# Performance work log

Measured on AMD Instinct MI355X. Metric: run time of the kernel, lower is better.

## Reference

```python
import jax, jax.numpy as jnp
import numpy as np

B, N, D = 4, 1024, 512
H, Dv, Dq = 8, 64, 64
NUM_BUCKETS = 64
LN_EPS = 1e-5


def setup_inputs() -> dict:
    key = jax.random.key(0)
    ks = jax.random.split(key, 10)
    x = jax.random.normal(ks[0], (B, N, D), dtype=jnp.float32)
    ts = jnp.sort(jax.random.randint(ks[1], (B, N), 0, 1_000_000), axis=1).astype(jnp.int64)
    cm = jnp.triu(jnp.ones((N, N), dtype=bool), k=1)  # causal: mask j > i
    pm = jnp.zeros((B, N), dtype=bool)                # no padding
    uvqk = 0.02 * jax.random.normal(ks[2], (D, 2 * H * Dv + 2 * H * Dq), dtype=jnp.float32)
    lim = float(np.sqrt(6.0 / (H * Dv + D)))
    o_w = jax.random.uniform(ks[3], (H * Dv, D), minval=-lim, maxval=lim, dtype=jnp.float32)
    o_b = jnp.zeros((D,), dtype=jnp.float32)
    ln_x_w = jnp.ones((D,), jnp.float32); ln_x_b = jnp.zeros((D,), jnp.float32)
    ln_a_w = jnp.ones((H * Dv,), jnp.float32); ln_a_b = jnp.zeros((H * Dv,), jnp.float32)
    ts_w = 0.02 * jax.random.normal(ks[4], (NUM_BUCKETS + 1,), dtype=jnp.float32)
    pos_w = 0.02 * jax.random.normal(ks[5], (2 * N - 1,), dtype=jnp.float32)
    return {"x": x, "ts": ts, "cm": cm, "pm": pm, "uvqk": uvqk, "o_w": o_w, "o_b": o_b,
            "ln_x_w": ln_x_w, "ln_x_b": ln_x_b, "ln_a_w": ln_a_w, "ln_a_b": ln_a_b,
            "ts_w": ts_w, "pos_w": pos_w}


def _layernorm(x, w, b):
    m = jnp.mean(x, axis=-1, keepdims=True)
    v = jnp.mean(jnp.square(x - m), axis=-1, keepdims=True)
    return (x - m) / jnp.sqrt(v + LN_EPS) * w + b


def _rel_bias(ts, ts_w, pos_w):
    # positional part: pb[i, j] = pos_w[j - i + N - 1], shape [N, N]
    idx = jnp.arange(N)
    pb = pos_w[idx[None, :] - idx[:, None] + N - 1]
    # bucketed time part
    ext = jnp.concatenate([ts, ts[:, N - 1:N]], axis=1)           # [B, N+1]
    diff = ext[:, 1:, None] - ext[:, None, :-1]                   # [B, N, N]
    logd = jnp.log(jnp.maximum(jnp.abs(diff), 1).astype(jnp.float32))
    bk = jnp.clip((logd / 0.301).astype(jnp.int32), 0, NUM_BUCKETS)
    return pb[None] + ts_w[bk]                                    # [B, N, N]


def reference(x, ts, cm, pm, uvqk, o_w, o_b, ln_x_w, ln_x_b, ln_a_w, ln_a_b, ts_w, pos_w):
    nx = _layernorm(x, ln_x_w, ln_x_b)                            # [B, N, D]
    out = jax.nn.silu(jnp.einsum('bnd,de->bne', nx, uvqk))        # [B, N, 2HDv+2HDq]
    u, v, q, k = jnp.split(out, [H * Dv, 2 * H * Dv, 2 * H * Dv + H * Dq], axis=-1)
    q = q.reshape(B, N, H, Dq)
    k = k.reshape(B, N, H, Dq)
    v = v.reshape(B, N, H, Dv)
    qk = jnp.einsum('bihd,bjhd->bhij', q, k) + _rel_bias(ts, ts_w, pos_w)[:, None]
    qk = jax.nn.silu(qk) / N
    qk = jnp.where(cm[None, None], 0.0, qk)          # causal mask
    qk = jnp.where(pm[:, None, None, :], 0.0, qk)    # padding mask on keys
    ao = jnp.einsum('bhij,bjhd->bihd', qk, v).reshape(B, N, H * Dv)
    ao = _layernorm(ao, ln_a_w, ln_a_b)
    u = u.reshape(B, N, H * Dv)
    y = (u * ao) @ o_w + o_b + x
    return jnp.where(pm[:, :, None], 0.0, y)
```

## Files before the change

kernel.cpp:

```cpp
#include <hip/hip_runtime.h>
#include <hip/hip_bf16.h>


typedef __attribute__((ext_vector_type(8))) short short8;
typedef __attribute__((ext_vector_type(4))) short bf4;
typedef __attribute__((ext_vector_type(4))) float floatx4;
typedef __attribute__((ext_vector_type(16))) float floatx16;

#define MFMA_BF16 __builtin_amdgcn_mfma_f32_16x16x32_bf16
#define MFMA32 __builtin_amdgcn_mfma_f32_32x32x16_bf16

static __device__ __forceinline__ short f2bf(float f) {
  unsigned u = __builtin_bit_cast(unsigned, f);
  u = (u + 0x7fffu + ((u >> 16) & 1u)) >> 16;
  return (short)u;
}
static __device__ __forceinline__ unsigned pk_bf16(float a, float b) {
  __hip_bfloat162 h = __float22bfloat162_rn(float2{a, b});
  unsigned u;
  __builtin_memcpy(&u, &h, 4);
  return u;
}
static __device__ __forceinline__ short lo16(unsigned u) { return (short)(u & 0xffffu); }
static __device__ __forceinline__ short hi16(unsigned u) { return (short)(u >> 16); }
static __device__ __forceinline__ float bf2f(short s) {
  unsigned u = ((unsigned)(unsigned short)s) << 16;
  return __builtin_bit_cast(float, u);
}
static __device__ __forceinline__ float bflo(unsigned u) {
  return __builtin_bit_cast(float, u << 16);
}
static __device__ __forceinline__ float bfhi(unsigned u) {
  return __builtin_bit_cast(float, u & 0xffff0000u);
}
static __device__ __forceinline__ float silu_f(float x) {
  return x / (1.f + __expf(-x));
}
static __device__ __forceinline__ void permswap(unsigned& a, unsigned& b) {
#if __has_builtin(__builtin_amdgcn_permlane32_swap)
  typedef __attribute__((ext_vector_type(2))) unsigned uint2v;
  uint2v r = __builtin_amdgcn_permlane32_swap(a, b, false, false);
  a = r[0];
  b = r[1];
#else
  asm volatile("v_permlane32_swap_b32 %0, %1" : "+v"(a), "+v"(b));
#endif
}
static __device__ __forceinline__ short8 mk8(unsigned a, unsigned b, unsigned c,
                                             unsigned d) {
  union {
    unsigned u[4];
    short8 s;
  } r;
  r.u[0] = a;
  r.u[1] = b;
  r.u[2] = c;
  r.u[3] = d;
  return r.s;
}
static __device__ __forceinline__ void gl_lds16(const void* g, void* l) {
  __builtin_amdgcn_global_load_lds(
      (const __attribute__((address_space(1))) unsigned int*)g,
      (__attribute__((address_space(3))) unsigned int*)l, 16, 0, 0);
}

__global__ __launch_bounds__(256) void prep_kernel(
    const float* __restrict__ x, const int* __restrict__ ts,
    const float* __restrict__ uvqk, const float* __restrict__ o_w,
    const float* __restrict__ ln_x_w, const float* __restrict__ ln_x_b,
    const float* __restrict__ ts_w, const float* __restrict__ pos_w,
    short* __restrict__ nx, short* __restrict__ uvqk_t,
    short* __restrict__ o_wt, short* __restrict__ bias) {
  __shared__ float tile[32][33];
  const int id = blockIdx.x;
  const int t = threadIdx.x;
  if (id < 4096) {
    const int b = id >> 10, i = id & 1023;
    int ie = i + 1; if (ie > 1023) ie = 1023;
    const int tse = ts[(b << 10) + ie];
    const int j0 = t * 4;
    int4 tj = *(const int4*)&ts[(b << 10) + j0];
    const int* tjp = (const int*)&tj;
    float ov[4];
#pragma unroll
    for (int e = 0; e < 4; ++e) {
      int dt = tse - tjp[e];
      float ad = fabsf((float)dt);
      if (ad < 1.f) ad = 1.f;
      int bkt = (int)(__logf(ad) * (1.f / 0.301f));
      if (bkt > 64) bkt = 64;
      ov[e] = pos_w[j0 + e - i + 1023] + ts_w[bkt];
    }
    uint2 o2 = {pk_bf16(ov[0], ov[1]), pk_bf16(ov[2], ov[3])};
    *(uint2*)&bias[((size_t)id << 10) + j0] = o2;
  } else if (id < 5120) {
    const int lane = t & 63;
    const int row = ((id - 4096) << 2) + (t >> 6);
    const int c0 = lane * 8;
    const float* xr = x + (size_t)row * 512;
    float v[8];
    *(float4*)&v[0] = *(const float4*)(xr + c0);
    *(float4*)&v[4] = *(const float4*)(xr + c0 + 4);
    float s = 0.f, sq = 0.f;
#pragma unroll
    for (int e = 0; e < 8; ++e) { s += v[e]; sq += v[e] * v[e]; }
#pragma unroll
    for (int off = 32; off > 0; off >>= 1) {
      s += __shfl_xor(s, off);
      sq += __shfl_xor(sq, off);
    }
    float m = s * (1.f / 512.f);
    float var = sq * (1.f / 512.f) - m * m;
    float rinv = rsqrtf(var + 1e-5f);
    float wv[8], bv[8];
    *(float4*)&wv[0] = *(const float4*)(ln_x_w + c0);
    *(float4*)&wv[4] = *(const float4*)(ln_x_w + c0 + 4);
    *(float4*)&bv[0] = *(const float4*)(ln_x_b + c0);
    *(float4*)&bv[4] = *(const float4*)(ln_x_b + c0 + 4);
    float o[8];
#pragma unroll
    for (int e = 0; e < 8; ++e) o[e] = (v[e] - m) * rinv * wv[e] + bv[e];
    uint4 o4 = {pk_bf16(o[0], o[1]), pk_bf16(o[2], o[3]),
                pk_bf16(o[4], o[5]), pk_bf16(o[6], o[7])};
    *(uint4*)(nx + (size_t)row * 512 + c0) = o4;
  } else {
    const float* src; short* dst; int R, C, bc, br;
    if (id < 6144) {
      int idm = id - 5120;
      src = uvqk; dst = uvqk_t; R = 512; C = 2048;
      bc = (idm & 63) * 32; br = (idm >> 6) * 32;
    } else {
      int idm = id - 6144;
      src = o_w; dst = o_wt; R = 512; C = 512;
      bc = (idm & 15) * 32; br = (idm >> 4) * 32;
    }
    const int c = t & 31, r0 = t >> 5;
#pragma unroll
    for (int p = 0; p < 4; ++p) {
      int r = r0 + p * 8;
      tile[r][c] = src[(size_t)(br + r) * C + bc + c];
    }
    __syncthreads();
#pragma unroll
    for (int p = 0; p < 4; ++p) {
      int r = r0 + p * 8;
      dst[(size_t)(bc + r) * R + br + c] = f2bf(tile[c][r]);
    }
  }
}

__global__ __launch_bounds__(256) void gemm1_kernel(
    const short* __restrict__ A, const short* __restrict__ Bt,
    short* __restrict__ u_buf, short* __restrict__ vt_buf,
    short* __restrict__ q_buf, short* __restrict__ k_buf) {
  __shared__ __align__(16) short As[2][128 * 32];
  __shared__ __align__(16) short Bs[2][128 * 32];
  const int t = threadIdx.x;
  const int lane = t & 63, w = t >> 6;
  const int quad = lane >> 4, l15 = lane & 15;
  const int m0 = blockIdx.x * 128, n0 = blockIdx.y * 128;
  const int wm = (w & 1) * 64, wn = (w >> 1) * 64;
  const int lr = lane >> 2, lc = (lane & 3) * 8;
  floatx4 acc[4][4];
#pragma unroll
  for (int i = 0; i < 4; ++i)
#pragma unroll
    for (int j = 0; j < 4; ++j) acc[i][j] = (floatx4){0.f, 0.f, 0.f, 0.f};

  for (int k0 = 0; k0 < 512; k0 += 64) {
    __syncthreads();
#pragma unroll
    for (int c = 0; c < 2; ++c)
#pragma unroll
      for (int p = 0; p < 2; ++p) {
        int ra = w * 32 + p * 16;
        gl_lds16(&A[(size_t)(m0 + ra + lr) * 512 + k0 + c * 32 + lc], &As[c][ra * 32]);
        gl_lds16(&Bt[(size_t)(n0 + ra + lr) * 512 + k0 + c * 32 + lc], &Bs[c][ra * 32]);
      }
    __syncthreads();
#pragma unroll
    for (int c = 0; c < 2; ++c) {
      short8 af[4], bfr[4];
#pragma unroll
      for (int mi = 0; mi < 4; ++mi) af[mi] = *(const short8*)&As[c][(wm + mi * 16 + l15) * 32 + quad * 8];
#pragma unroll
      for (int ni = 0; ni < 4; ++ni) bfr[ni] = *(const short8*)&Bs[c][(wn + ni * 16 + l15) * 32 + quad * 8];
#pragma unroll
      for (int mi = 0; mi < 4; ++mi)
#pragma unroll
        for (int ni = 0; ni < 4; ++ni)
          acc[mi][ni] = MFMA_BF16(af[mi], bfr[ni], acc[mi][ni], 0, 0, 0);
    }
  }
  const int seg = n0 >> 9, cbase = n0 & 511;
  if (seg == 0) {
#pragma unroll
    for (int mi = 0; mi < 4; ++mi)
#pragma unroll
      for (int ni = 0; ni < 4; ++ni) {
        int row0 = m0 + wm + mi * 16 + quad * 4;
        int c = cbase + wn + ni * 16 + l15;
        float v0 = silu_f(acc[mi][ni][0]), v1 = silu_f(acc[mi][ni][1]);
        float v2 = silu_f(acc[mi][ni][2]), v3 = silu_f(acc[mi][ni][3]);
        unsigned pa = pk_bf16(v0, v1), pb = pk_bf16(v2, v3);
        u_buf[(size_t)row0 * 512 + c] = lo16(pa);
        u_buf[(size_t)(row0 + 1) * 512 + c] = hi16(pa);
        u_buf[(size_t)(row0 + 2) * 512 + c] = lo16(pb);
        u_buf[(size_t)(row0 + 3) * 512 + c] = hi16(pb);
      }
  } else if (seg == 1) {
#pragma unroll
    for (int mi = 0; mi < 4; ++mi)
#pragma unroll
      for (int ni = 0; ni < 4; ++ni) {
        int c = cbase + wn + ni * 16 + l15;
        int h = c >> 6, d = c & 63;
        int row0 = m0 + wm + mi * 16 + quad * 4;
        int b_ = row0 >> 10, nb = row0 & 1023;
        float v0 = silu_f(acc[mi][ni][0]) * (1.f / 1024.f);
        float v1 = silu_f(acc[mi][ni][1]) * (1.f / 1024.f);
        float v2 = silu_f(acc[mi][ni][2]) * (1.f / 1024.f);
        float v3 = silu_f(acc[mi][ni][3]) * (1.f / 1024.f);
        uint2 sv = {pk_bf16(v0, v1), pk_bf16(v2, v3)};
        *(uint2*)&vt_buf[(((size_t)(b_ * 8 + h) * 64 + d) << 10) + nb] = sv;
      }
  } else {
    short* dst = (seg == 2) ? q_buf : k_buf;
#pragma unroll
    for (int mi = 0; mi < 4; ++mi)
#pragma unroll
      for (int ni = 0; ni < 4; ++ni) {
        int row0 = m0 + wm + mi * 16 + quad * 4;
        int c = cbase + wn + ni * 16 + l15;
        int b_ = row0 >> 10, nb = row0 & 1023;
        size_t base = ((((size_t)(b_ * 8 + (c >> 6))) << 10) + nb) * 64 + (c & 63);
        float v0 = silu_f(acc[mi][ni][0]), v1 = silu_f(acc[mi][ni][1]);
        float v2 = silu_f(acc[mi][ni][2]), v3 = silu_f(acc[mi][ni][3]);
        unsigned pa = pk_bf16(v0, v1), pb = pk_bf16(v2, v3);
        dst[base] = lo16(pa);
        dst[base + 64] = hi16(pa);
        dst[base + 128] = lo16(pb);
        dst[base + 192] = hi16(pb);
      }
  }
}

__global__ __launch_bounds__(256, 3) void attn_kernel(
    const short* __restrict__ q_buf, const short* __restrict__ k_buf,
    const short* __restrict__ vt_buf, const short* __restrict__ bias_buf,
    short* __restrict__ ao_part) {
  __shared__ __align__(16) short k_s[64][72];
  __shared__ __align__(16) short vt_s[64][72];

  const int t = threadIdx.x;
  const int lane = t & 63, w = t >> 6;
  const int l31 = lane & 31, hh = lane >> 5, h8 = hh * 8;
  const int bh = blockIdx.x, y4 = blockIdx.y, jh = blockIdx.z;
  const int b = bh >> 3, hd = bh & 7;
  const short* qh = q_buf + (size_t)bh * 65536;
  const short* kh = k_buf + (size_t)bh * 65536;
  const short* vth = vt_buf + (size_t)bh * 65536;
  const int sr = t >> 2, sc = (t & 3) * 16;

#pragma unroll
  for (int half = 0; half < 2; ++half) {
    const int it = half ? (7 - y4) : y4;
    const int i0 = it * 128;
    const int iw0 = i0 + w * 32;
    const int ig = iw0 + l31;
    const int jtmax = 2 * it + 1;
    short8 qf[4];
#pragma unroll
    for (int kk = 0; kk < 4; ++kk)
      qf[kk] = *(const short8*)&qh[(size_t)ig * 64 + kk * 16 + h8];
    const short* brow = bias_buf + (((size_t)(b * 1024 + ig)) << 10);
    float4 kr0, kr1, vr0, vr1;
    {
      int j0 = jh * 64;
      kr0 = *(const float4*)&kh[(size_t)(j0 + sr) * 64 + sc];
      kr1 = *(const float4*)&kh[(size_t)(j0 + sr) * 64 + sc + 8];
      vr0 = *(const float4*)&vth[(size_t)sr * 1024 + j0 + sc];
      vr1 = *(const float4*)&vth[(size_t)sr * 1024 + j0 + sc + 8];
    }
    floatx16 ao0, ao1;
#pragma unroll
    for (int r = 0; r < 16; ++r) { ao0[r] = 0.f; ao1[r] = 0.f; }

    auto sub_tile = [&](const uint2* bw, int jcol, int jb, bool needmask) {
      floatx16 s;
#pragma unroll
      for (int g = 0; g < 4; ++g) {
        s[4 * g + 0] = bflo(bw[g].x);
        s[4 * g + 1] = bfhi(bw[g].x);
        s[4 * g + 2] = bflo(bw[g].y);
        s[4 * g + 3] = bfhi(bw[g].y);
      }
#pragma unroll
      for (int kk = 0; kk < 4; ++kk) {
        short8 ak = *(const short8*)&k_s[jcol + l31][kk * 16 + h8];
        s = MFMA32(ak, qf[kk], s, 0, 0, 0);
      }
      float p[16];
#pragma unroll
      for (int r = 0; r < 16; ++r) {
        float xv = s[r];
        float pv = xv / (1.f + __expf(-xv));
        if (needmask) {
          int jg = jb + hh * 4 + (r & 3) + 8 * (r >> 2);
          if (jg > ig) pv = 0.f;
        }
        p[r] = pv;
      }
      unsigned X0 = pk_bf16(p[0], p[1]), Y0 = pk_bf16(p[2], p[3]);
      unsigned X1 = pk_bf16(p[4], p[5]), Y1 = pk_bf16(p[6], p[7]);
      unsigned X2 = pk_bf16(p[8], p[9]), Y2 = pk_bf16(p[10], p[11]);
      unsigned X3 = pk_bf16(p[12], p[13]), Y3 = pk_bf16(p[14], p[15]);
      permswap(X0, X1);
      permswap(Y0, Y1);
      permswap(X2, X3);
      permswap(Y2, Y3);
      short8 pa0 = mk8(X0, Y0, X1, Y1);
      short8 pa1 = mk8(X2, Y2, X3, Y3);
#pragma unroll
      for (int c = 0; c < 2; ++c) {
        short8 pa = c ? pa1 : pa0;
        short8 bv0 = *(const short8*)&vt_s[l31][jcol + c * 16 + h8];
        short8 bv1 = *(const short8*)&vt_s[32 + l31][jcol + c * 16 + h8];
        ao0 = MFMA32(pa, bv0, ao0, 0, 0, 0);
        ao1 = MFMA32(pa, bv1, ao1, 0, 0, 0);
      }
    };

    for (int jt = jh; jt <= jtmax; jt += 4) {
      const int j0a = jt * 64, j0b = j0a + 32;
      const bool live_a = (j0a <= iw0 + 31);
      const bool live_b = (j0b <= iw0 + 31);
      const bool mask_a = live_a && (j0a + 31 > iw0);
      const bool mask_b = live_b && (j0b + 31 > iw0);
      uint2 bwa[4], bwb[4];
      if (live_a) {
#pragma unroll
        for (int g = 0; g < 4; ++g)
          bwa[g] = *(const uint2*)&brow[j0a + g * 8 + hh * 4];
      }
      if (live_b) {
#pragma unroll
        for (int g = 0; g < 4; ++g)
          bwb[g] = *(const uint2*)&brow[j0b + g * 8 + hh * 4];
      }
      __syncthreads();
      *(float4*)&k_s[sr][sc] = kr0;
      *(float4*)&k_s[sr][sc + 8] = kr1;
      *(float4*)&vt_s[sr][sc] = vr0;
      *(float4*)&vt_s[sr][sc + 8] = vr1;
      {
        int jn = (jt + 4 <= jtmax) ? jt + 4 : jt;
        int jn0 = jn * 64;
        kr0 = *(const float4*)&kh[(size_t)(jn0 + sr) * 64 + sc];
        kr1 = *(const float4*)&kh[(size_t)(jn0 + sr) * 64 + sc + 8];
        vr0 = *(const float4*)&vth[(size_t)sr * 1024 + jn0 + sc];
        vr1 = *(const float4*)&vth[(size_t)sr * 1024 + jn0 + sc + 8];
      }
      __syncthreads();
      if (!live_a) continue;
      __builtin_amdgcn_s_setprio(1);
      sub_tile(bwa, 0, j0a, mask_a);
      if (live_b) sub_tile(bwb, 32, j0b, mask_b);
      __builtin_amdgcn_s_setprio(0);
    }
    short* aod = ao_part + (size_t)jh * 2097152;
#pragma unroll
    for (int r = 0; r < 16; ++r) {
      int gi = iw0 + (r & 3) + 8 * (r >> 2) + 4 * hh;
      size_t base = ((size_t)(b * 1024 + gi)) * 512 + hd * 64 + l31;
      aod[base] = f2bf(ao0[r]);
      aod[base + 32] = f2bf(ao1[r]);
    }
  }
}

__global__ __launch_bounds__(256) void ln_mul_kernel(
    const short* __restrict__ ao_part, const short* __restrict__ u,
    const float* __restrict__ w_, const float* __restrict__ b_,
    short* __restrict__ g) {
  const int lane = threadIdx.x & 63;
  const int row = (blockIdx.x << 2) + (threadIdx.x >> 6);
  const int c0 = lane * 8;
  short8 a0 = *(const short8*)(ao_part + (size_t)row * 512 + c0);
  short8 a1 = *(const short8*)(ao_part + 2097152 + (size_t)row * 512 + c0);
  short8 a2 = *(const short8*)(ao_part + 4194304 + (size_t)row * 512 + c0);
  short8 a3 = *(const short8*)(ao_part + 6291456 + (size_t)row * 512 + c0);
  float v[8];
#pragma unroll
  for (int e = 0; e < 8; ++e)
    v[e] = (bf2f(a0[e]) + bf2f(a1[e])) + (bf2f(a2[e]) + bf2f(a3[e]));
  float s = 0.f, sq = 0.f;
#pragma unroll
  for (int e = 0; e < 8; ++e) { s += v[e]; sq += v[e] * v[e]; }
#pragma unroll
  for (int off = 32; off > 0; off >>= 1) {
    s += __shfl_xor(s, off);
    sq += __shfl_xor(sq, off);
  }
  float m = s * (1.f / 512.f);
  float var = sq * (1.f / 512.f) - m * m;
  float rinv = rsqrtf(var + 1e-5f);
  float wv[8], bv[8];
  *(float4*)&wv[0] = *(const float4*)(w_ + c0);
  *(float4*)&wv[4] = *(const float4*)(w_ + c0 + 4);
  *(float4*)&bv[0] = *(const float4*)(b_ + c0);
  *(float4*)&bv[4] = *(const float4*)(b_ + c0 + 4);
  short8 uv = *(const short8*)(u + (size_t)row * 512 + c0);
  float o[8];
#pragma unroll
  for (int e = 0; e < 8; ++e)
    o[e] = bf2f(uv[e]) * ((v[e] - m) * rinv * wv[e] + bv[e]);
  uint4 o4 = {pk_bf16(o[0], o[1]), pk_bf16(o[2], o[3]),
              pk_bf16(o[4], o[5]), pk_bf16(o[6], o[7])};
  *(uint4*)(g + (size_t)row * 512 + c0) = o4;
}

__global__ __launch_bounds__(256) void gemm2_kernel(
    const short* __restrict__ G, const short* __restrict__ Wt,
    const float* __restrict__ o_b, const float* __restrict__ x,
    float* __restrict__ out) {
  __shared__ __align__(16) short As[2][64 * 32];
  __shared__ __align__(16) short Bs[2][64 * 32];
  const int t = threadIdx.x;
  const int lane = t & 63, w = t >> 6;
  const int quad = lane >> 4, l15 = lane & 15;
  const int m0 = blockIdx.x * 64, n0 = blockIdx.y * 64;
  const int lr = lane >> 2, lc = (lane & 3) * 8;
  floatx4 acc[4];
#pragma unroll
  for (int j = 0; j < 4; ++j) acc[j] = (floatx4){0.f, 0.f, 0.f, 0.f};

  for (int k0 = 0; k0 < 512; k0 += 64) {
    __syncthreads();
#pragma unroll
    for (int c = 0; c < 2; ++c) {
      int ra = w * 16;
      gl_lds16(&G[(size_t)(m0 + ra + lr) * 512 + k0 + c * 32 + lc], &As[c][ra * 32]);
      gl_lds16(&Wt[(size_t)(n0 + ra + lr) * 512 + k0 + c * 32 + lc], &Bs[c][ra * 32]);
    }
    __syncthreads();
#pragma unroll
    for (int c = 0; c < 2; ++c) {
      short8 af = *(const short8*)&As[c][(w * 16 + l15) * 32 + quad * 8];
#pragma unroll
      for (int ni = 0; ni < 4; ++ni) {
        short8 bfr = *(const short8*)&Bs[c][(ni * 16 + l15) * 32 + quad * 8];
        acc[ni] = MFMA_BF16(af, bfr, acc[ni], 0, 0, 0);
      }
    }
  }
#pragma unroll
  for (int ni = 0; ni < 4; ++ni)
#pragma unroll
    for (int r = 0; r < 4; ++r) {
      int row = m0 + w * 16 + quad * 4 + r;
      int c = n0 + ni * 16 + l15;
      out[(size_t)row * 512 + c] = acc[ni][r] + o_b[c] + x[(size_t)row * 512 + c];
    }
}

extern "C" void kernel_launch(void* const* d_in, const int* in_sizes, int n_in,
                              void* d_out, int out_size, void* d_ws, size_t ws_size,
                              hipStream_t stream) {
  const float* x = (const float*)d_in[0];
  const int* ts = (const int*)d_in[1];
  const float* uvqk = (const float*)d_in[4];
  const float* o_w = (const float*)d_in[5];
  const float* o_b = (const float*)d_in[6];
  const float* ln_x_w = (const float*)d_in[7];
  const float* ln_x_b = (const float*)d_in[8];
  const float* ln_a_w = (const float*)d_in[9];
  const float* ln_a_b = (const float*)d_in[10];
  const float* ts_w = (const float*)d_in[11];
  const float* pos_w = (const float*)d_in[12];
  float* out = (float*)d_out;

  char* ws = (char*)d_ws;
  short* nx = (short*)(ws + 0);
  short* uvqk_t = (short*)(ws + 4194304);
  short* o_wt = (short*)(ws + 6291456);
  short* u_buf = (short*)(ws + 6815744);
  short* q_buf = (short*)(ws + 11010048);
  short* k_buf = (short*)(ws + 15204352);
  short* vt_buf = (short*)(ws + 19398656);
  short* bias_buf = (short*)(ws + 23592960);
  short* ao_part = (short*)(ws + 31981568);
  short* g_buf = nx;

  hipLaunchKernelGGL(prep_kernel, dim3(6400), dim3(256), 0, stream,
                     x, ts, uvqk, o_w, ln_x_w, ln_x_b, ts_w, pos_w,
                     nx, uvqk_t, o_wt, bias_buf);
  hipLaunchKernelGGL(gemm1_kernel, dim3(32, 16), dim3(256), 0, stream, nx, uvqk_t, u_buf, vt_buf, q_buf, k_buf);
  hipLaunchKernelGGL(attn_kernel, dim3(32, 4, 4), dim3(256), 0, stream, q_buf, k_buf, vt_buf, bias_buf, ao_part);
  hipLaunchKernelGGL(ln_mul_kernel, dim3(1024), dim3(256), 0, stream, ao_part, u_buf, ln_a_w, ln_a_b, g_buf);
  hipLaunchKernelGGL(gemm2_kernel, dim3(64, 8), dim3(256), 0, stream, g_buf, o_wt, o_b, x, out);
}
```

Baseline: 147.4 us.

## Transpose relative-bias layout so attention bias loads coalesce across lanes

The prep kernel now writes the bias matrix transposed (indexed by key then query), and the attention kernel reads it with per-element 16-bit loads where consecutive lanes touch consecutive query positions. The intent is to turn strided row-wise bias reads into coalesced accesses. In exchange each lane issues 16 scalar loads instead of 4 vector loads, and the bias is added after the MFMA rather than used as the accumulator seed.

```diff
diff --git a/kernel.cpp b/kernel.cpp
--- a/kernel.cpp
+++ b/kernel.cpp
@@ -26,12 +26,6 @@
 static __device__ __forceinline__ float bf2f(short s) {
   unsigned u = ((unsigned)(unsigned short)s) << 16;
   return __builtin_bit_cast(float, u);
-}
-static __device__ __forceinline__ float bflo(unsigned u) {
-  return __builtin_bit_cast(float, u << 16);
-}
-static __device__ __forceinline__ float bfhi(unsigned u) {
-  return __builtin_bit_cast(float, u & 0xffff0000u);
 }
 static __device__ __forceinline__ float silu_f(float x) {
   return x / (1.f + __expf(-x));
@@ -75,24 +69,25 @@
   const int id = blockIdx.x;
   const int t = threadIdx.x;
   if (id < 4096) {
-    const int b = id >> 10, i = id & 1023;
-    int ie = i + 1; if (ie > 1023) ie = 1023;
-    const int tse = ts[(b << 10) + ie];
-    const int j0 = t * 4;
-    int4 tj = *(const int4*)&ts[(b << 10) + j0];
-    const int* tjp = (const int*)&tj;
+    const int b = id >> 10, j = id & 1023;
+    const int tsj = ts[(b << 10) + j];
+    const int i0 = t * 4;
+    int4 ti = *(const int4*)&ts[(b << 10) + i0];
+    const int* tip = (const int*)&ti;
+    int tlast = ts[(b << 10) + ((i0 + 4 <= 1023) ? i0 + 4 : 1023)];
+    int te[4] = {tip[1], tip[2], tip[3], tlast};
     float ov[4];
 #pragma unroll
     for (int e = 0; e < 4; ++e) {
-      int dt = tse - tjp[e];
+      int dt = te[e] - tsj;
       float ad = fabsf((float)dt);
       if (ad < 1.f) ad = 1.f;
       int bkt = (int)(__logf(ad) * (1.f / 0.301f));
       if (bkt > 64) bkt = 64;
-      ov[e] = pos_w[j0 + e - i + 1023] + ts_w[bkt];
+      ov[e] = pos_w[j - (i0 + e) + 1023] + ts_w[bkt];
     }
     uint2 o2 = {pk_bf16(ov[0], ov[1]), pk_bf16(ov[2], ov[3])};
-    *(uint2*)&bias[((size_t)id << 10) + j0] = o2;
+    *(uint2*)&bias[((size_t)id << 10) + i0] = o2;
   } else if (id < 5120) {
     const int lane = t & 63;
     const int row = ((id - 4096) << 2) + (t >> 6);
@@ -260,6 +255,7 @@
   const short* qh = q_buf + (size_t)bh * 65536;
   const short* kh = k_buf + (size_t)bh * 65536;
   const short* vth = vt_buf + (size_t)bh * 65536;
+  const short* btb = bias_buf + ((size_t)b << 20);
   const int sr = t >> 2, sc = (t & 3) * 16;
 
 #pragma unroll
@@ -273,7 +269,6 @@
 #pragma unroll
     for (int kk = 0; kk < 4; ++kk)
       qf[kk] = *(const short8*)&qh[(size_t)ig * 64 + kk * 16 + h8];
-    const short* brow = bias_buf + (((size_t)(b * 1024 + ig)) << 10);
     float4 kr0, kr1, vr0, vr1;
     {
       int j0 = jh * 64;
@@ -286,15 +281,11 @@
 #pragma unroll
     for (int r = 0; r < 16; ++r) { ao0[r] = 0.f; ao1[r] = 0.f; }
 
-    auto sub_tile = [&](const uint2* bw, int jcol, int jb, bool needmask) {
+    auto sub_tile = [&](const unsigned short* ba, int jcol, int jb,
+                        bool needmask) {
       floatx16 s;
 #pragma unroll
-      for (int g = 0; g < 4; ++g) {
-        s[4 * g + 0] = bflo(bw[g].x);
-        s[4 * g + 1] = bfhi(bw[g].x);
-        s[4 * g + 2] = bflo(bw[g].y);
-        s[4 * g + 3] = bfhi(bw[g].y);
-      }
+      for (int r = 0; r < 16; ++r) s[r] = 0.f;
 #pragma unroll
       for (int kk = 0; kk < 4; ++kk) {
         short8 ak = *(const short8*)&k_s[jcol + l31][kk * 16 + h8];
@@ -303,7 +294,7 @@
       float p[16];
 #pragma unroll
       for (int r = 0; r < 16; ++r) {
-        float xv = s[r];
+        float xv = s[r] + bf2f((short)ba[r]);
         float pv = xv / (1.f + __expf(-xv));
         if (needmask) {
           int jg = jb + hh * 4 + (r & 3) + 8 * (r >> 2);
@@ -337,16 +328,18 @@
       const bool live_b = (j0b <= iw0 + 31);
       const bool mask_a = live_a && (j0a + 31 > iw0);
       const bool mask_b = live_b && (j0b + 31 > iw0);
-      uint2 bwa[4], bwb[4];
+      unsigned short ba[16], bb[16];
       if (live_a) {
-#pragma unroll
-        for (int g = 0; g < 4; ++g)
-          bwa[g] = *(const uint2*)&brow[j0a + g * 8 + hh * 4];
+        const short* bp = btb + (((size_t)(j0a + 4 * hh)) << 10) + iw0 + l31;
+#pragma unroll
+        for (int r = 0; r < 16; ++r)
+          ba[r] = (unsigned short)bp[((size_t)((r & 3) + 8 * (r >> 2))) << 10];
       }
       if (live_b) {
-#pragma unroll
-        for (int g = 0; g < 4; ++g)
-          bwb[g] = *(const uint2*)&brow[j0b + g * 8 + hh * 4];
+        const short* bp = btb + (((size_t)(j0b + 4 * hh)) << 10) + iw0 + l31;
+#pragma unroll
+        for (int r = 0; r < 16; ++r)
+          bb[r] = (unsigned short)bp[((size_t)((r & 3) + 8 * (r >> 2))) << 10];
       }
       __syncthreads();
       *(float4*)&k_s[sr][sc] = kr0;
@@ -364,8 +357,8 @@
       __syncthreads();
       if (!live_a) continue;
       __builtin_amdgcn_s_setprio(1);
-      sub_tile(bwa, 0, j0a, mask_a);
-      if (live_b) sub_tile(bwb, 32, j0b, mask_b);
+      sub_tile(ba, 0, j0a, mask_a);
+      if (live_b) sub_tile(bb, 32, j0b, mask_b);
       __builtin_amdgcn_s_setprio(0);
     }
     short* aod = ao_part + (size_t)jh * 2097152;
```

Result: no change. 147.5 us (+0.1%).

## Split attention key tiles across warp pairs with LDS reduction, halve query tile

Applied to the files above, without the earlier changes.

The attention kernel now uses 64-row query tiles instead of 128 and splits each 64-key tile between two warp pairs. Each warp handles a 32x32 query/key sub-tile, and the two partial outputs are summed through a new shared-memory reduction buffer before the store. The grid doubles along y and launch bounds target 4 blocks per CU, which increases parallelism and spreads the causal work more evenly. In exchange it adds an LDS reduction, extra barriers and more K/V staging per query row, since each K/V tile is now loaded for fewer queries.

```diff
diff --git a/kernel.cpp b/kernel.cpp
--- a/kernel.cpp
+++ b/kernel.cpp
@@ -245,17 +245,19 @@
   }
 }
 
-__global__ __launch_bounds__(256, 3) void attn_kernel(
+__global__ __launch_bounds__(256, 4) void attn_kernel(
     const short* __restrict__ q_buf, const short* __restrict__ k_buf,
     const short* __restrict__ vt_buf, const short* __restrict__ bias_buf,
     short* __restrict__ ao_part) {
   __shared__ __align__(16) short k_s[64][72];
   __shared__ __align__(16) short vt_s[64][72];
+  __shared__ __align__(16) float red_s[2][32][64];
 
   const int t = threadIdx.x;
   const int lane = t & 63, w = t >> 6;
   const int l31 = lane & 31, hh = lane >> 5, h8 = hh * 8;
-  const int bh = blockIdx.x, y4 = blockIdx.y, jh = blockIdx.z;
+  const int wi = w & 1, wj = w >> 1;
+  const int bh = blockIdx.x, pair = blockIdx.y, jh = blockIdx.z;
   const int b = bh >> 3, hd = bh & 7;
   const short* qh = q_buf + (size_t)bh * 65536;
   const short* kh = k_buf + (size_t)bh * 65536;
@@ -264,11 +266,10 @@
 
 #pragma unroll
   for (int half = 0; half < 2; ++half) {
-    const int it = half ? (7 - y4) : y4;
-    const int i0 = it * 128;
-    const int iw0 = i0 + w * 32;
+    const int it = half ? (15 - pair) : pair;
+    const int i0 = it * 64;
+    const int iw0 = i0 + wi * 32;
     const int ig = iw0 + l31;
-    const int jtmax = 2 * it + 1;
     short8 qf[4];
 #pragma unroll
     for (int kk = 0; kk < 4; ++kk)
@@ -286,7 +287,32 @@
 #pragma unroll
     for (int r = 0; r < 16; ++r) { ao0[r] = 0.f; ao1[r] = 0.f; }
 
-    auto sub_tile = [&](const uint2* bw, int jcol, int jb, bool needmask) {
+    for (int jt = jh; jt <= it; jt += 4) {
+      const int j0w = jt * 64 + wj * 32;
+      const bool live = (j0w <= iw0 + 31);
+      const bool needmask = live && (j0w + 31 > iw0);
+      uint2 bw[4];
+      if (live) {
+#pragma unroll
+        for (int g = 0; g < 4; ++g)
+          bw[g] = *(const uint2*)&brow[j0w + g * 8 + hh * 4];
+      }
+      __syncthreads();
+      *(float4*)&k_s[sr][sc] = kr0;
+      *(float4*)&k_s[sr][sc + 8] = kr1;
+      *(float4*)&vt_s[sr][sc] = vr0;
+      *(float4*)&vt_s[sr][sc + 8] = vr1;
+      {
+        int jn = (jt + 4 <= it) ? jt + 4 : jt;
+        int jn0 = jn * 64;
+        kr0 = *(const float4*)&kh[(size_t)(jn0 + sr) * 64 + sc];
+        kr1 = *(const float4*)&kh[(size_t)(jn0 + sr) * 64 + sc + 8];
+        vr0 = *(const float4*)&vth[(size_t)sr * 1024 + jn0 + sc];
+        vr1 = *(const float4*)&vth[(size_t)sr * 1024 + jn0 + sc + 8];
+      }
+      __syncthreads();
+      if (!live) continue;
+      __builtin_amdgcn_s_setprio(1);
       floatx16 s;
 #pragma unroll
       for (int g = 0; g < 4; ++g) {
@@ -297,7 +323,7 @@
       }
 #pragma unroll
       for (int kk = 0; kk < 4; ++kk) {
-        short8 ak = *(const short8*)&k_s[jcol + l31][kk * 16 + h8];
+        short8 ak = *(const short8*)&k_s[wj * 32 + l31][kk * 16 + h8];
         s = MFMA32(ak, qf[kk], s, 0, 0, 0);
       }
       float p[16];
@@ -306,7 +332,7 @@
         float xv = s[r];
         float pv = xv / (1.f + __expf(-xv));
         if (needmask) {
-          int jg = jb + hh * 4 + (r & 3) + 8 * (r >> 2);
+          int jg = j0w + hh * 4 + (r & 3) + 8 * (r >> 2);
           if (jg > ig) pv = 0.f;
         }
         p[r] = pv;
@@ -324,57 +350,35 @@
 #pragma unroll
       for (int c = 0; c < 2; ++c) {
         short8 pa = c ? pa1 : pa0;
-        short8 bv0 = *(const short8*)&vt_s[l31][jcol + c * 16 + h8];
-        short8 bv1 = *(const short8*)&vt_s[32 + l31][jcol + c * 16 + h8];
+        short8 bv0 = *(const short8*)&vt_s[l31][wj * 32 + c * 16 + h8];
+        short8 bv1 = *(const short8*)&vt_s[32 + l31][wj * 32 + c * 16 + h8];
         ao0 = MFMA32(pa, bv0, ao0, 0, 0, 0);
         ao1 = MFMA32(pa, bv1, ao1, 0, 0, 0);
       }
-    };
-
-    for (int jt = jh; jt <= jtmax; jt += 4) {
-      const int j0a = jt * 64, j0b = j0a + 32;
-      const bool live_a = (j0a <= iw0 + 31);
-      const bool live_b = (j0b <= iw0 + 31);
-      const bool mask_a = live_a && (j0a + 31 > iw0);
-      const bool mask_b = live_b && (j0b + 31 > iw0);
-      uint2 bwa[4], bwb[4];
-      if (live_a) {
-#pragma unroll
-        for (int g = 0; g < 4; ++g)
-          bwa[g] = *(const uint2*)&brow[j0a + g * 8 + hh * 4];
-      }
-      if (live_b) {
-#pragma unroll
-        for (int g = 0; g < 4; ++g)
-          bwb[g] = *(const uint2*)&brow[j0b + g * 8 + hh * 4];
-      }
-      __syncthreads();
-      *(float4*)&k_s[sr][sc] = kr0;
-      *(float4*)&k_s[sr][sc + 8] = kr1;
-      *(float4*)&vt_s[sr][sc] = vr0;
-      *(float4*)&vt_s[sr][sc + 8] = vr1;
-      {
-        int jn = (jt + 4 <= jtmax) ? jt + 4 : jt;
-        int jn0 = jn * 64;
-        kr0 = *(const float4*)&kh[(size_t)(jn0 + sr) * 64 + sc];
-        kr1 = *(const float4*)&kh[(size_t)(jn0 + sr) * 64 + sc + 8];
-        vr0 = *(const float4*)&vth[(size_t)sr * 1024 + jn0 + sc];
-        vr1 = *(const float4*)&vth[(size_t)sr * 1024 + jn0 + sc + 8];
-      }
-      __syncthreads();
-      if (!live_a) continue;
-      __builtin_amdgcn_s_setprio(1);
-      sub_tile(bwa, 0, j0a, mask_a);
-      if (live_b) sub_tile(bwb, 32, j0b, mask_b);
       __builtin_amdgcn_s_setprio(0);
     }
-    short* aod = ao_part + (size_t)jh * 2097152;
-#pragma unroll
-    for (int r = 0; r < 16; ++r) {
-      int gi = iw0 + (r & 3) + 8 * (r >> 2) + 4 * hh;
-      size_t base = ((size_t)(b * 1024 + gi)) * 512 + hd * 64 + l31;
-      aod[base] = f2bf(ao0[r]);
-      aod[base + 32] = f2bf(ao1[r]);
+    __syncthreads();
+    if (wj == 1) {
+#pragma unroll
+      for (int r = 0; r < 16; ++r) {
+        int il = (r & 3) + 8 * (r >> 2) + 4 * hh;
+        red_s[wi][il][l31] = ao0[r];
+        red_s[wi][il][32 + l31] = ao1[r];
+      }
+    }
+    __syncthreads();
+    if (wj == 0) {
+      short* aod = ao_part + (size_t)jh * 2097152;
+#pragma unroll
+      for (int r = 0; r < 16; ++r) {
+        int il = (r & 3) + 8 * (r >> 2) + 4 * hh;
+        float a0 = ao0[r] + red_s[wi][il][l31];
+        float a1 = ao1[r] + red_s[wi][il][32 + l31];
+        int gi = iw0 + il;
+        size_t base = ((size_t)(b * 1024 + gi)) * 512 + hd * 64 + l31;
+        aod[base] = f2bf(a0);
+        aod[base + 32] = f2bf(a1);
+      }
     }
   }
 }
@@ -496,7 +500,7 @@
                      x, ts, uvqk, o_w, ln_x_w, ln_x_b, ts_w, pos_w,
                      nx, uvqk_t, o_wt, bias_buf);
   hipLaunchKernelGGL(gemm1_kernel, dim3(32, 16), dim3(256), 0, stream, nx, uvqk_t, u_buf, vt_buf, q_buf, k_buf);
-  hipLaunchKernelGGL(attn_kernel, dim3(32, 4, 4), dim3(256), 0, stream, q_buf, k_buf, vt_buf, bias_buf, ao_part);
+  hipLaunchKernelGGL(attn_kernel, dim3(32, 8, 4), dim3(256), 0, stream, q_buf, k_buf, vt_buf, bias_buf, ao_part);
   hipLaunchKernelGGL(ln_mul_kernel, dim3(1024), dim3(256), 0, stream, ao_part, u_buf, ln_a_w, ln_a_b, g_buf);
   hipLaunchKernelGGL(gemm2_kernel, dim3(64, 8), dim3(256), 0, stream, g_buf, o_wt, o_b, x, out);
 }
```

New measurement: 144.5 us. Within noise of the previous version (-1.9%).
